# Performance work log

Measured on AMD Instinct MI355X. Metric: run time of the kernel, lower is better.

## Reference

```python
import jax, jax.numpy as jnp
import numpy as np

S, B, H, E, L, V = 64, 64, 512, 512, 2, 32000


def setup_inputs() -> dict:
    key = jax.random.key(0)
    ks = jax.random.split(key, 10)
    k = 1.0 / np.sqrt(H)
    return {
        "tokens": jax.random.randint(ks[0], (S, B), 0, V),
        "hidden": jnp.zeros((L, B, H), jnp.float32),
        "emb": jax.random.uniform(ks[1], (V, E), jnp.float32, -0.1, 0.1),
        "Wr": jax.random.uniform(ks[2], (L, E + H, H), jnp.float32, -k, k),
        "br": jax.random.uniform(ks[3], (L, H), jnp.float32, -k, k),
        "Wz": jax.random.uniform(ks[4], (L, E + H, H), jnp.float32, -k, k),
        "bz": jax.random.uniform(ks[5], (L, H), jnp.float32, -k, k),
        "Wh": jax.random.uniform(ks[6], (L, E + H, H), jnp.float32, -k, k),
        "bh": jax.random.uniform(ks[7], (L, H), jnp.float32, -k, k),
        "Wout": jax.random.uniform(ks[8], (H, V), jnp.float32, -0.1, 0.1),
        "bout": jnp.zeros((V,), jnp.float32),
    }


def reference(tokens, hidden, emb, Wr, br, Wz, bz, Wh, bh, Wout, bout):
    # tokens: [S,B] int; hidden: [L,B,H]
    x = emb[tokens]  # [S,B,E]  (dropout is identity: dp_keep_prob=1)

    def step(h, x_t):  # h: [L,B,H], x_t: [B,E]
        inp = x_t
        new_h = []
        for l in range(L):
            cat = jnp.concatenate([inp, h[l]], axis=-1)  # [B, E+H]
            r = jax.nn.sigmoid(cat @ Wr[l] + br[l])
            z = jax.nn.sigmoid(cat @ Wz[l] + bz[l])
            cat_h = jnp.concatenate([inp, r * h[l]], axis=-1)
            hh = jnp.tanh(cat_h @ Wh[l] + bh[l])
            nh = (1.0 - z) * h[l] + z * hh
            new_h.append(nh)
            inp = nh
        h_new = jnp.stack(new_h)  # [L,B,H]
        logits_t = inp @ Wout + bout  # [B,V]
        return h_new, logits_t

    hidden_final, logits = jax.lax.scan(step, hidden, x)
    return logits, hidden_final  # [S,B,V], [L,B,H]
```

## Files before the change

### kernel.cpp

```cpp
#include <hip/hip_runtime.h>
#include <hip/hip_bf16.h>
#include <math.h>

#define S_ 64
#define B_ 64
#define H_ 512
#define E_ 512
#define L_ 2
#define V_ 32000

#define SB_   (S_*B_)
#define SBE_  (S_*B_*E_)
#define SBH_  (S_*B_*H_)
#define BH_   (B_*H_)

__global__ __launch_bounds__(256) void embed_k(const int* __restrict__ tok,
                                               const float* __restrict__ emb,
                                               float* __restrict__ x) {
    int idx = blockIdx.x * 256 + threadIdx.x;
    int e4 = idx & (E_/4 - 1);
    int sb = idx >> 7;
    int tk = tok[sb];
    *(float4*)(x + (size_t)sb * E_ + e4 * 4) =
        *(const float4*)(emb + (size_t)tk * E_ + e4 * 4);
}

__global__ __launch_bounds__(256) void gemm_bias(
    const float* __restrict__ A, int lda,
    const float* __restrict__ W, int ldw,
    const float* __restrict__ bias,
    float* __restrict__ C, int ldc,
    int K) {
    __shared__ float As[16][68];
    __shared__ float Bs[16][68];

    const int tid = threadIdx.x;
    const int tx = tid & 15;
    const int ty = tid >> 4;
    const int n0 = blockIdx.x * 64;
    const int m0 = blockIdx.y * 64;

    float acc[4][4] = {};

    for (int k0 = 0; k0 < K; k0 += 16) {
        {
            int i  = tid >> 2;
            int j4 = tid & 3;
            const float4 av = *(const float4*)(A + (size_t)(m0 + i) * lda + k0 + j4 * 4);
            As[j4 * 4 + 0][i] = av.x;
            As[j4 * 4 + 1][i] = av.y;
            As[j4 * 4 + 2][i] = av.z;
            As[j4 * 4 + 3][i] = av.w;
        }
        {
            int r  = tid >> 4;
            int c4 = tid & 15;
            *(float4*)(&Bs[r][c4 * 4]) =
                *(const float4*)(W + (size_t)(k0 + r) * ldw + n0 + c4 * 4);
        }
        __syncthreads();
        #pragma unroll
        for (int kk = 0; kk < 16; kk++) {
            float4 a4 = *(float4*)(&As[kk][ty * 4]);
            float4 b4 = *(float4*)(&Bs[kk][tx * 4]);
            acc[0][0] += a4.x * b4.x; acc[0][1] += a4.x * b4.y; acc[0][2] += a4.x * b4.z; acc[0][3] += a4.x * b4.w;
            acc[1][0] += a4.y * b4.x; acc[1][1] += a4.y * b4.y; acc[1][2] += a4.y * b4.z; acc[1][3] += a4.y * b4.w;
            acc[2][0] += a4.z * b4.x; acc[2][1] += a4.z * b4.y; acc[2][2] += a4.z * b4.z; acc[2][3] += a4.z * b4.w;
            acc[3][0] += a4.w * b4.x; acc[3][1] += a4.w * b4.y; acc[3][2] += a4.w * b4.z; acc[3][3] += a4.w * b4.w;
        }
        __syncthreads();
    }

    float4 bv = *(const float4*)(bias + n0 + tx * 4);
    #pragma unroll
    for (int i = 0; i < 4; i++) {
        int row = m0 + ty * 4 + i;
        float4 out;
        out.x = acc[i][0] + bv.x;
        out.y = acc[i][1] + bv.y;
        out.z = acc[i][2] + bv.z;
        out.w = acc[i][3] + bv.w;
        *(float4*)(C + (size_t)row * ldc + n0 + tx * 4) = out;
    }
}

__device__ __forceinline__ float sigmoidf_(float xv) {
    float e = __expf(-fabsf(xv));
    float s = 1.f / (1.f + e);
    return xv >= 0.f ? s : 1.f - s;
}

__global__ __launch_bounds__(256) void rz_step(
    const float* __restrict__ Pr_t, const float* __restrict__ Pz_t,
    const float* __restrict__ Wr_hid, const float* __restrict__ Wz_hid,
    const float* __restrict__ h_prev,
    float* __restrict__ zbuf, float* __restrict__ rhbuf) {
    __shared__ float hs[64][132];
    const int bid = blockIdx.x;
    const int g = bid >> 5;
    const int ct = bid & 31;
    const int tid = threadIdx.x;
    const int c = ct * 16 + (tid & 15);
    const int bg = tid >> 4;

    const float* Wg = g ? Wz_hid : Wr_hid;
    const float* P  = g ? Pz_t   : Pr_t;

    float acc[4] = {0.f, 0.f, 0.f, 0.f};

    for (int kk = 0; kk < H_; kk += 128) {
        #pragma unroll
        for (int q = 0; q < 8; q++) {
            int idx = q * 256 + tid;
            int row = idx >> 5;
            int c4  = idx & 31;
            *(float4*)(&hs[row][c4 * 4]) =
                *(const float4*)(h_prev + row * H_ + kk + c4 * 4);
        }
        __syncthreads();
        const float* Wp = Wg + (size_t)kk * H_ + c;
        #pragma unroll 4
        for (int k = 0; k < 128; k++) {
            float w = Wp[(size_t)k * H_];
            #pragma unroll
            for (int i = 0; i < 4; i++)
                acc[i] += w * hs[bg * 4 + i][k];
        }
        __syncthreads();
    }

    #pragma unroll
    for (int i = 0; i < 4; i++) {
        int b = bg * 4 + i;
        float pre = P[b * H_ + c] + acc[i];
        float v = sigmoidf_(pre);
        if (g == 0) rhbuf[b * H_ + c] = v * h_prev[b * H_ + c];
        else        zbuf[b * H_ + c]  = v;
    }
}

__global__ __launch_bounds__(256) void hh_step(
    const float* __restrict__ Ph_t,
    const float* __restrict__ Wh_hid,
    const float* __restrict__ rh,
    const float* __restrict__ h_prev,
    const float* __restrict__ zbuf,
    float* __restrict__ h_out) {
    __shared__ float hs[64][132];
    const int ct = blockIdx.x;
    const int tid = threadIdx.x;
    const int c = ct * 16 + (tid & 15);
    const int bg = tid >> 4;

    float acc[4] = {0.f, 0.f, 0.f, 0.f};

    for (int kk = 0; kk < H_; kk += 128) {
        #pragma unroll
        for (int q = 0; q < 8; q++) {
            int idx = q * 256 + tid;
            int row = idx >> 5;
            int c4  = idx & 31;
            *(float4*)(&hs[row][c4 * 4]) =
                *(const float4*)(rh + row * H_ + kk + c4 * 4);
        }
        __syncthreads();
        const float* Wp = Wh_hid + (size_t)kk * H_ + c;
        #pragma unroll 4
        for (int k = 0; k < 128; k++) {
            float w = Wp[(size_t)k * H_];
            #pragma unroll
            for (int i = 0; i < 4; i++)
                acc[i] += w * hs[bg * 4 + i][k];
        }
        __syncthreads();
    }

    #pragma unroll
    for (int i = 0; i < 4; i++) {
        int b = bg * 4 + i;
        float pre = Ph_t[b * H_ + c] + acc[i];
        float hhv = tanhf(pre);
        float z = zbuf[b * H_ + c];
        float h = h_prev[b * H_ + c];
        h_out[b * H_ + c] = (1.f - z) * h + z * hhv;
    }
}

extern "C" void kernel_launch(void* const* d_in, const int* in_sizes, int n_in,
                              void* d_out, int out_size, void* d_ws, size_t ws_size,
                              hipStream_t stream) {
    const int*   tokens = (const int*)  d_in[0];
    const float* hidden = (const float*)d_in[1];
    const float* emb    = (const float*)d_in[2];
    const float* Wr     = (const float*)d_in[3];
    const float* br     = (const float*)d_in[4];
    const float* Wz     = (const float*)d_in[5];
    const float* bz     = (const float*)d_in[6];
    const float* Wh     = (const float*)d_in[7];
    const float* bh     = (const float*)d_in[8];
    const float* Wout   = (const float*)d_in[9];
    const float* bout   = (const float*)d_in[10];

    float* out = (float*)d_out;
    float* out_hidden = out + (size_t)SB_ * V_;

    float* ws = (float*)d_ws;
    float* x     = ws;
    float* hseq1 = x + SBE_;
    float* hseq2 = hseq1 + SBH_;
    float* Pr    = hseq2 + SBH_;
    float* Pz    = Pr + SBH_;
    float* Ph    = Pz + SBH_;
    float* zbuf  = Ph + SBH_;
    float* rhbuf = zbuf + BH_;

    embed_k<<<SBE_ / 4 / 256, 256, 0, stream>>>(tokens, emb, x);

    const int WL = (E_ + H_) * H_;
    const float* layer_in[2] = {x, hseq1};
    float* hseqs[2] = {hseq1, hseq2};

    for (int l = 0; l < L_; l++) {
        const float* A = layer_in[l];
        const float* Wr_l = Wr + (size_t)l * WL;
        const float* Wz_l = Wz + (size_t)l * WL;
        const float* Wh_l = Wh + (size_t)l * WL;

        dim3 gpre(H_ / 64, SB_ / 64);
        gemm_bias<<<gpre, 256, 0, stream>>>(A, E_, Wr_l, H_, br + l * H_, Pr, H_, E_);
        gemm_bias<<<gpre, 256, 0, stream>>>(A, E_, Wz_l, H_, bz + l * H_, Pz, H_, E_);
        gemm_bias<<<gpre, 256, 0, stream>>>(A, E_, Wh_l, H_, bh + l * H_, Ph, H_, E_);

        const float* Wr_hid = Wr_l + (size_t)E_ * H_;
        const float* Wz_hid = Wz_l + (size_t)E_ * H_;
        const float* Wh_hid = Wh_l + (size_t)E_ * H_;

        for (int t = 0; t < S_; t++) {
            const float* h_prev = (t == 0) ? (hidden + (size_t)l * BH_)
                                           : (hseqs[l] + (size_t)(t - 1) * BH_);
            rz_step<<<64, 256, 0, stream>>>(Pr + (size_t)t * BH_, Pz + (size_t)t * BH_,
                                            Wr_hid, Wz_hid, h_prev, zbuf, rhbuf);
            hh_step<<<32, 256, 0, stream>>>(Ph + (size_t)t * BH_, Wh_hid, rhbuf,
                                            h_prev, zbuf, hseqs[l] + (size_t)t * BH_);
        }

        hipMemcpyAsync(out_hidden + (size_t)l * BH_, hseqs[l] + (size_t)(S_ - 1) * BH_,
                       (size_t)BH_ * sizeof(float), hipMemcpyDeviceToDevice, stream);
    }

    dim3 glog(V_ / 64, SB_ / 64);
    gemm_bias<<<glog, 256, 0, stream>>>(hseq2, H_, Wout, V_, bout, out, V_, H_);
}
```

Measured before the change: 9.193 ms.

## Compute output logits GEMM with split-fp16 MFMA instead of fp32 SIMT

Replaces the fp32 SIMT logits GEMM with an MFMA fp16 kernel. Activations and Wout are split into hi/lo fp16 parts packed along an extended K of 1536, which emulates near-fp32 precision with three fp16 products. The kernel uses direct global-to-LDS loads with a swizzled layout and 128x128 tiles. This adds cast kernels, including transposing and casting the full Wout on every call, and the scaled hi/lo splitting carries some precision risk.

```diff
diff --git a/kernel.cpp b/kernel.cpp
--- a/kernel.cpp
+++ b/kernel.cpp
@@ -13,6 +13,11 @@
 #define SBE_  (S_*B_*E_)
 #define SBH_  (S_*B_*H_)
 #define BH_   (B_*H_)
+#define KP_   1536
+
+typedef _Float16 f16x8 __attribute__((ext_vector_type(8)));
+typedef _Float16 f16x4 __attribute__((ext_vector_type(4)));
+typedef float    f32x4 __attribute__((ext_vector_type(4)));
 
 __global__ __launch_bounds__(256) void embed_k(const int* __restrict__ tok,
                                                const float* __restrict__ emb,
@@ -183,6 +188,146 @@
         float z = zbuf[b * H_ + c];
         float h = h_prev[b * H_ + c];
         h_out[b * H_ + c] = (1.f - z) * h + z * hhv;
+    }
+}
+
+__global__ __launch_bounds__(256) void castA_k(const float* __restrict__ in,
+                                               _Float16* __restrict__ A2) {
+    int idx = blockIdx.x * 256 + threadIdx.x;
+    int m = idx >> 7;
+    int q = idx & 127;
+    float4 xv = *(const float4*)(in + (size_t)m * H_ + q * 4);
+    float xs[4] = {xv.x, xv.y, xv.z, xv.w};
+    f16x4 hi, lo, sc;
+    #pragma unroll
+    for (int i = 0; i < 4; i++) {
+        _Float16 ah = (_Float16)xs[i];
+        float ahf = (float)ah;
+        hi[i] = ah;
+        lo[i] = (_Float16)((xs[i] - ahf) * 32.0f);
+        sc[i] = (_Float16)(ahf * 0.0625f);
+    }
+    _Float16* row = A2 + (size_t)m * KP_ + q * 4;
+    *(f16x4*)(row)        = hi;
+    *(f16x4*)(row + 512)  = lo;
+    *(f16x4*)(row + 1024) = sc;
+}
+
+__global__ __launch_bounds__(256) void castB_k(const float* __restrict__ W,
+                                               _Float16* __restrict__ Bt) {
+    __shared__ float ws[64][68];
+    const int v0 = blockIdx.x * 64;
+    const int h0 = blockIdx.y * 64;
+    const int tid = threadIdx.x;
+
+    #pragma unroll
+    for (int q = 0; q < 4; q++) {
+        int idx = q * 256 + tid;
+        int h  = idx >> 4;
+        int v4 = idx & 15;
+        *(float4*)(&ws[h][v4 * 4]) =
+            *(const float4*)(W + (size_t)(h0 + h) * V_ + v0 + v4 * 4);
+    }
+    __syncthreads();
+
+    const int v  = tid >> 2;
+    const int hq = tid & 3;
+    #pragma unroll
+    for (int j = 0; j < 2; j++) {
+        int hb = j * 32 + hq * 8;
+        f16x8 hi, lo, sc;
+        #pragma unroll
+        for (int i = 0; i < 8; i++) {
+            float wv = ws[hb + i][v];
+            _Float16 bh = (_Float16)wv;
+            float bhf = (float)bh;
+            hi[i] = bh;
+            sc[i] = (_Float16)(bhf * 0.03125f);
+            lo[i] = (_Float16)((wv - bhf) * 16.0f);
+        }
+        _Float16* row = Bt + (size_t)(v0 + v) * KP_ + h0 + hb;
+        *(f16x8*)(row)        = hi;
+        *(f16x8*)(row + 512)  = sc;
+        *(f16x8*)(row + 1024) = lo;
+    }
+}
+
+__global__ __launch_bounds__(256) void gemm_logits(
+    const _Float16* __restrict__ Ag,
+    const _Float16* __restrict__ Bg,
+    const float* __restrict__ bias,
+    float* __restrict__ C) {
+    __shared__ __align__(16) _Float16 As[128 * 64];
+    __shared__ __align__(16) _Float16 Bs[128 * 64];
+
+    const int tid  = threadIdx.x;
+    const int lane = tid & 63;
+    const int w    = tid >> 6;
+    const int n0   = blockIdx.x * 128;
+    const int m0   = blockIdx.y * 128;
+    const int wm   = (w >> 1) * 64;
+    const int wn   = (w & 1) * 64;
+
+    f32x4 acc[4][4];
+    #pragma unroll
+    for (int i = 0; i < 4; i++)
+        #pragma unroll
+        for (int j = 0; j < 4; j++)
+            acc[i][j] = (f32x4){0.f, 0.f, 0.f, 0.f};
+
+    const int grow  = lane >> 3;
+    const int gslot = (lane & 7) ^ grow;
+
+    for (int kt = 0; kt < KP_ / 64; ++kt) {
+        const int k0 = kt * 64;
+        #pragma unroll
+        for (int q = 0; q < 4; ++q) {
+            int ch  = w * 4 + q;
+            int row = ch * 8 + grow;
+            const _Float16* ga = Ag + (size_t)(m0 + row) * KP_ + k0 + gslot * 8;
+            const _Float16* gb = Bg + (size_t)(n0 + row) * KP_ + k0 + gslot * 8;
+            __builtin_amdgcn_global_load_lds(
+                (const __attribute__((address_space(1))) void*)ga,
+                (__attribute__((address_space(3))) void*)(As + ch * 512), 16, 0, 0);
+            __builtin_amdgcn_global_load_lds(
+                (const __attribute__((address_space(1))) void*)gb,
+                (__attribute__((address_space(3))) void*)(Bs + ch * 512), 16, 0, 0);
+        }
+        __syncthreads();
+
+        #pragma unroll
+        for (int ks = 0; ks < 2; ++ks) {
+            f16x8 af[4], bf[4];
+            #pragma unroll
+            for (int i = 0; i < 4; ++i) {
+                int arow  = wm + i * 16 + (lane & 15);
+                int aslot = (ks * 4 + (lane >> 4)) ^ (arow & 7);
+                af[i] = *(const f16x8*)(As + arow * 64 + aslot * 8);
+                int brow  = wn + i * 16 + (lane & 15);
+                int bslot = (ks * 4 + (lane >> 4)) ^ (brow & 7);
+                bf[i] = *(const f16x8*)(Bs + brow * 64 + bslot * 8);
+            }
+            #pragma unroll
+            for (int mi = 0; mi < 4; ++mi)
+                #pragma unroll
+                for (int nj = 0; nj < 4; ++nj)
+                    acc[mi][nj] = __builtin_amdgcn_mfma_f32_16x16x32_f16(
+                        af[mi], bf[nj], acc[mi][nj], 0, 0, 0);
+        }
+        __syncthreads();
+    }
+
+    #pragma unroll
+    for (int nj = 0; nj < 4; ++nj) {
+        int col = n0 + wn + nj * 16 + (lane & 15);
+        float bv = bias[col];
+        #pragma unroll
+        for (int mi = 0; mi < 4; ++mi) {
+            int rb = m0 + wm + mi * 16 + (lane >> 4) * 4;
+            #pragma unroll
+            for (int j = 0; j < 4; ++j)
+                C[(size_t)(rb + j) * V_ + col] = acc[mi][nj][j] + bv;
+        }
     }
 }
 
@@ -213,8 +358,12 @@
     float* Ph    = Pz + SBH_;
     float* zbuf  = Ph + SBH_;
     float* rhbuf = zbuf + BH_;
+    _Float16* A2 = (_Float16*)(rhbuf + BH_);
+    _Float16* Bt = A2 + (size_t)SB_ * KP_;
 
     embed_k<<<SBE_ / 4 / 256, 256, 0, stream>>>(tokens, emb, x);
+
+    castB_k<<<dim3(V_ / 64, H_ / 64), 256, 0, stream>>>(Wout, Bt);
 
     const int WL = (E_ + H_) * H_;
     const float* layer_in[2] = {x, hseq1};
@@ -248,6 +397,7 @@
                        (size_t)BH_ * sizeof(float), hipMemcpyDeviceToDevice, stream);
     }
 
-    dim3 glog(V_ / 64, SB_ / 64);
-    gemm_bias<<<glog, 256, 0, stream>>>(hseq2, H_, Wout, V_, bout, out, V_, H_);
-}
+    castA_k<<<SBE_ / 4 / 256, 256, 0, stream>>>(hseq2, A2);
+
+    gemm_logits<<<dim3(V_ / 128, SB_ / 128), 256, 0, stream>>>(A2, Bt, bout, out);
+}
```

After: 7.663 ms. 16.6% less time.
